# Kernel optimization log

Hardware: AMD Instinct MI355X
Metric: run time of the kernel (lower is better)

Reference implementation:

```python
import jax, jax.numpy as jnp
import numpy as np

B, S, E, H = 256, 512, 128, 256


def setup_inputs() -> dict:
    key = jax.random.key(0)
    ks = jax.random.split(key, 20)
    s = lambda *sh: 1.0 / np.sqrt(sh[-1])
    inp = jax.random.uniform(ks[0], (B, S, 2), dtype=jnp.float32)
    W_emb = jax.random.normal(ks[1], (E, 2), jnp.float32) * 0.5
    dec_input = jax.random.normal(ks[2], (E,), jnp.float32) * 0.1
    # encoder LSTM (input E -> hidden H), pytorch gate order i,f,g,o
    enc_Wih = jax.random.normal(ks[3], (4 * H, E), jnp.float32) * s(E)
    enc_Whh = jax.random.normal(ks[4], (4 * H, H), jnp.float32) * s(H)
    enc_bih = jnp.zeros((4 * H,), jnp.float32)
    enc_bhh = jnp.zeros((4 * H,), jnp.float32)
    # process block LSTM (input E -> hidden H)
    pb_Wih = jax.random.normal(ks[5], (4 * H, E), jnp.float32) * s(E)
    pb_Whh = jax.random.normal(ks[6], (4 * H, H), jnp.float32) * s(H)
    pb_bih = jnp.zeros((4 * H,), jnp.float32)
    pb_bhh = jnp.zeros((4 * H,), jnp.float32)
    # attention: W_q Linear(H,H), W_ref Conv1d(H,H,1), v vector
    Wq = jax.random.normal(ks[7], (H, H), jnp.float32) * s(H)
    bq = jnp.zeros((H,), jnp.float32)
    Wref = jax.random.normal(ks[8], (H, H), jnp.float32) * s(H)
    bref = jnp.zeros((H,), jnp.float32)
    V = jax.random.normal(ks[9], (H,), jnp.float32) * s(H)
    # decoder: Linear(H,H,bias=False) -> ReLU -> Linear(H,1,bias=False)
    Wd1 = jax.random.normal(ks[10], (H, H), jnp.float32) * s(H)
    Wd2 = jax.random.normal(ks[11], (1, H), jnp.float32) * s(H)
    return dict(inp=inp, W_emb=W_emb, dec_input=dec_input,
                enc_Wih=enc_Wih, enc_Whh=enc_Whh, enc_bih=enc_bih, enc_bhh=enc_bhh,
                pb_Wih=pb_Wih, pb_Whh=pb_Whh, pb_bih=pb_bih, pb_bhh=pb_bhh,
                Wq=Wq, bq=bq, Wref=Wref, bref=bref, V=V, Wd1=Wd1, Wd2=Wd2)


def _lstm_step(Whh):
    def step(carry, x_proj):
        h, c = carry
        g = x_proj + h @ Whh.T  # [B,4H]
        i, f, gg, o = jnp.split(g, 4, axis=-1)
        c = jax.nn.sigmoid(f) * c + jax.nn.sigmoid(i) * jnp.tanh(gg)
        h = jax.nn.sigmoid(o) * jnp.tanh(c)
        return (h, c), h
    return step


def reference(inp, W_emb, dec_input,
              enc_Wih, enc_Whh, enc_bih, enc_bhh,
              pb_Wih, pb_Whh, pb_bih, pb_bhh,
              Wq, bq, Wref, bref, V, Wd1, Wd2):
    b, seq, _ = inp.shape
    hdim = enc_Whh.shape[1]
    emb = inp @ W_emb.T  # [B,S,E]

    # ---- encoder LSTM over the sequence ----
    x_proj = emb @ enc_Wih.T + enc_bih + enc_bhh  # [B,S,4H]
    h0 = jnp.zeros((b, hdim), inp.dtype)
    c0 = jnp.zeros((b, hdim), inp.dtype)
    (h, c), hs = jax.lax.scan(_lstm_step(enc_Whh), (h0, c0),
                              jnp.swapaxes(x_proj, 0, 1))
    enc_out = jnp.swapaxes(hs, 0, 1)  # [B,S,H]

    # ---- process block: seq steps of single-step LSTM with constant input ----
    xp = dec_input @ pb_Wih.T + pb_bih + pb_bhh  # [4H]
    xp = jnp.broadcast_to(xp, (b, xp.shape[0]))
    step = _lstm_step(pb_Whh)
    (h, c), _ = jax.lax.scan(lambda carry, _: (step(carry, xp)[0], None),
                             (h, c), None, length=seq)

    # ---- attention (glimpse) with final hidden; inner iter loop is idempotent ----
    ref = enc_out @ Wref.T + bref            # [B,S,H]  (Conv1d kernel=1)
    q = h @ Wq.T + bq                        # [B,H]
    u = jnp.tanh(ref + q[:, None, :]) @ V    # [B,S]
    align = jax.nn.softmax(u, axis=-1)
    g_l = jnp.einsum('bs,bsh->bh', align, enc_out)  # glimpse [B,H]

    # ---- decoder head ----
    out = (jax.nn.relu(g_l @ Wd1.T)) @ Wd2.T  # [B,1]
    return out.squeeze(-1)
```

## Files before the change

### kernel.cpp

```cpp
#include <hip/hip_runtime.h>

#define B_ 256
#define S_ 512
#define E_ 128
#define H_ 256
#define FH_ 1024
#define HROW 264

typedef __bf16 bf16x8 __attribute__((ext_vector_type(8)));
typedef float f32x4 __attribute__((ext_vector_type(4)));
typedef unsigned short u16x4 __attribute__((ext_vector_type(4)));
typedef unsigned short u16x8 __attribute__((ext_vector_type(8)));
typedef unsigned long long u64_;

__device__ __forceinline__ unsigned short f2bf(float f) {
  union { float f; unsigned int u; } a; a.f = f;
  unsigned int u = a.u;
  u += 0x7fffu + ((u >> 16) & 1u);
  return (unsigned short)(u >> 16);
}
__device__ __forceinline__ float bf2f(unsigned short v) {
  union { unsigned int u; float f; } a; a.u = ((unsigned int)v) << 16;
  return a.f;
}
__device__ __forceinline__ float rcp_(float x) {
  float r;
  asm("v_rcp_f32 %0, %1" : "=v"(r) : "v"(x));
  return r;
}
__device__ __forceinline__ float sigm(float x) { return rcp_(1.f + __expf(-x)); }
__device__ __forceinline__ float tanh_(float x) {
  return 1.f - 2.f * rcp_(__expf(2.f * x) + 1.f);
}
__device__ __forceinline__ unsigned int cvt_pk_bf16(float lo, float hi) {
  unsigned int r;
  asm("v_cvt_pk_bf16_f32 %0, %1, %2" : "=v"(r) : "v"(lo), "v"(hi));
  return r;
}

#define OFF_ENC    ((size_t)0)
#define OFF_WHHE   ((size_t)67108864)
#define OFF_WHHP   ((size_t)67633152)
#define OFF_WREF   ((size_t)68157440)
#define OFF_MENC   ((size_t)68288512)
#define OFF_BIASE  ((size_t)68296704)
#define OFF_XPV    ((size_t)68300800)
#define OFF_FLAGS  ((size_t)68304896)
#define OFF_HX     ((size_t)68305920)
#define OFF_HFIN   ((size_t)68568064)
#define OFF_QBUF   ((size_t)68830208)
#define OFF_UBUF   ((size_t)69092352)

__global__ void k0_prep(const float* __restrict__ eWih, const float* __restrict__ eWhh,
                        const float* __restrict__ ebih, const float* __restrict__ ebhh,
                        const float* __restrict__ pWih, const float* __restrict__ pWhh,
                        const float* __restrict__ pbih, const float* __restrict__ pbhh,
                        const float* __restrict__ W_emb, const float* __restrict__ dec_in,
                        const float* __restrict__ Wref,
                        unsigned short* __restrict__ WhhE, unsigned short* __restrict__ WhhP,
                        unsigned short* __restrict__ Wrefb,
                        float* __restrict__ Menc, float* __restrict__ biasE,
                        float* __restrict__ xpv,
                        unsigned int* __restrict__ flags, float* __restrict__ ubuf) {
  int gid = blockIdx.x * blockDim.x + threadIdx.x;
  int NT = gridDim.x * blockDim.x;
  for (int i = gid; i < FH_ * H_; i += NT) {
    WhhE[i] = f2bf(eWhh[i]);
    WhhP[i] = f2bf(pWhh[i]);
  }
  for (int i = gid; i < H_ * H_; i += NT) Wrefb[i] = f2bf(Wref[i]);
  for (int i = gid; i < B_ * S_; i += NT) ubuf[i] = 0.f;
  if (gid < 256) flags[gid] = 0u;
  if (gid < FH_) {
    int n = gid;
    float m0 = 0.f, m1 = 0.f, xs = 0.f;
    for (int e = 0; e < E_; ++e) {
      float w = eWih[n * E_ + e];
      m0 += w * W_emb[e * 2 + 0];
      m1 += w * W_emb[e * 2 + 1];
      xs += pWih[n * E_ + e] * dec_in[e];
    }
    Menc[n * 2 + 0] = m0;
    Menc[n * 2 + 1] = m1;
    biasE[n] = ebih[n] + ebhh[n];
    xpv[n] = xs + pbih[n] + pbhh[n];
  }
}

__launch_bounds__(512)
__attribute__((amdgpu_waves_per_eu(2, 2)))
__global__ void k1_lstm(const float* __restrict__ inp,
                        const unsigned short* __restrict__ WhhE,
                        const unsigned short* __restrict__ WhhP,
                        const float* __restrict__ Menc, const float* __restrict__ biasE,
                        const float* __restrict__ xpv,
                        unsigned short* __restrict__ enc_out,
                        unsigned short* __restrict__ hx,
                        unsigned int* __restrict__ flags,
                        float* __restrict__ hfin) {
  __shared__ unsigned short hbuf[16 * HROW];
  __shared__ float xin[16][2];
  const int tid = threadIdx.x;
  const int wave = tid >> 6, lane = tid & 63, quad = lane >> 4, l16 = lane & 15;
  const int blk = blockIdx.x;
  const int grp = (blk & 7) | ((blk >> 4) << 3);
  const int half = (blk >> 3) & 1;
  const int kloc = (wave << 4) | l16;
  const int kcol = half * 128 + kloc;

  for (int i = tid; i < 16 * HROW; i += 512) hbuf[i] = 0;
  if (tid < 32) xin[tid >> 1][tid & 1] = inp[((grp * 16 + (tid >> 1)) * S_ + 0) * 2 + (tid & 1)];

  float c[4] = {0.f, 0.f, 0.f, 0.f};
  float hreg[4] = {0.f, 0.f, 0.f, 0.f};
  f32x4 W00, W01, W02, W03, W04, W05, W06, W07;
  f32x4 W10, W11, W12, W13, W14, W15, W16, W17;
  f32x4 W20, W21, W22, W23, W24, W25, W26, W27;
  f32x4 W30, W31, W32, W33, W34, W35, W36, W37;
  float m0c[4], m1c[4], bc[4];
  unsigned int* myflag = flags + grp * 2 + half;
  unsigned int* pflag = flags + grp * 2 + (1 - half);
  const f32x4 z4 = {0.f, 0.f, 0.f, 0.f};
  __syncthreads();

  int t = 0;
#pragma unroll 1
  for (int phase = 0; phase < 2; ++phase) {
    const unsigned short* W = phase ? WhhP : WhhE;
#define WLOAD(g)                                                        \
    {                                                                   \
      const unsigned short* wp = W + ((g) * 256 + kcol) * H_ + quad * 8; \
      W##g##0 = *(const f32x4*)(wp + 0 * 32);                           \
      W##g##1 = *(const f32x4*)(wp + 1 * 32);                           \
      W##g##2 = *(const f32x4*)(wp + 2 * 32);                           \
      W##g##3 = *(const f32x4*)(wp + 3 * 32);                           \
      W##g##4 = *(const f32x4*)(wp + 4 * 32);                           \
      W##g##5 = *(const f32x4*)(wp + 5 * 32);                           \
      W##g##6 = *(const f32x4*)(wp + 6 * 32);                           \
      W##g##7 = *(const f32x4*)(wp + 7 * 32);                           \
    }
    WLOAD(0) WLOAD(1) WLOAD(2) WLOAD(3)
#undef WLOAD
    asm volatile(""
                 : "+v"(W00), "+v"(W01), "+v"(W02), "+v"(W03),
                   "+v"(W04), "+v"(W05), "+v"(W06), "+v"(W07),
                   "+v"(W10), "+v"(W11), "+v"(W12), "+v"(W13),
                   "+v"(W14), "+v"(W15), "+v"(W16), "+v"(W17),
                   "+v"(W20), "+v"(W21), "+v"(W22), "+v"(W23),
                   "+v"(W24), "+v"(W25), "+v"(W26), "+v"(W27),
                   "+v"(W30), "+v"(W31), "+v"(W32), "+v"(W33),
                   "+v"(W34), "+v"(W35), "+v"(W36), "+v"(W37));
#pragma unroll
    for (int gg = 0; gg < 4; ++gg) {
      int n = gg * 256 + kcol;
      if (phase == 0) {
        m0c[gg] = Menc[n * 2 + 0]; m1c[gg] = Menc[n * 2 + 1]; bc[gg] = biasE[n];
      } else {
        m0c[gg] = 0.f; m1c[gg] = 0.f; bc[gg] = xpv[n];
      }
    }
#pragma unroll 1
    for (int step = 0; step < 512; ++step, ++t) {
      float xpre = 0.f;
      if (phase == 0 && tid < 32) {
        int sN = (step < 511) ? step + 1 : 511;
        xpre = inp[((grp * 16 + (tid >> 1)) * S_ + sN) * 2 + (tid & 1)];
      }
      f32x4 acc0 = z4, acc1 = z4, acc2 = z4, acc3 = z4;
#define MSTEP(kt)                                                              \
      {                                                                        \
        bf16x8 Af = *(const bf16x8*)(hbuf + l16 * HROW + kt * 32 + quad * 8);  \
        acc0 = __builtin_amdgcn_mfma_f32_16x16x32_bf16(                        \
            Af, __builtin_bit_cast(bf16x8, W0##kt), acc0, 0, 0, 0);            \
        acc1 = __builtin_amdgcn_mfma_f32_16x16x32_bf16(                        \
            Af, __builtin_bit_cast(bf16x8, W1##kt), acc1, 0, 0, 0);            \
        acc2 = __builtin_amdgcn_mfma_f32_16x16x32_bf16(                        \
            Af, __builtin_bit_cast(bf16x8, W2##kt), acc2, 0, 0, 0);            \
        acc3 = __builtin_amdgcn_mfma_f32_16x16x32_bf16(                        \
            Af, __builtin_bit_cast(bf16x8, W3##kt), acc3, 0, 0, 0);            \
      }
      MSTEP(0) MSTEP(1) MSTEP(2) MSTEP(3) MSTEP(4) MSTEP(5) MSTEP(6) MSTEP(7)
#undef MSTEP
      float hv[4];
#pragma unroll
      for (int r = 0; r < 4; ++r) {
        int bl = quad * 4 + r;
        float x0 = xin[bl][0], x1 = xin[bl][1];
        float gi = acc0[r] + x0 * m0c[0] + x1 * m1c[0] + bc[0];
        float gf = acc1[r] + x0 * m0c[1] + x1 * m1c[1] + bc[1];
        float gc = acc2[r] + x0 * m0c[2] + x1 * m1c[2] + bc[2];
        float go = acc3[r] + x0 * m0c[3] + x1 * m1c[3] + bc[3];
        float cn = sigm(gf) * c[r] + sigm(gi) * tanh_(gc);
        c[r] = cn;
        hv[r] = sigm(go) * tanh_(cn);
        hreg[r] = hv[r];
      }
      unsigned int pkA = cvt_pk_bf16(hv[0], hv[1]);
      unsigned int pkB = cvt_pk_bf16(hv[2], hv[3]);
      unsigned short hb[4];
      hb[0] = (unsigned short)pkA; hb[1] = (unsigned short)(pkA >> 16);
      hb[2] = (unsigned short)pkB; hb[3] = (unsigned short)(pkB >> 16);
      if (phase == 0) {
#pragma unroll
        for (int r = 0; r < 4; ++r)
          enc_out[(((size_t)(grp * 16 + quad * 4 + r) * S_ + step)) * H_ + kcol] = hb[r];
      }
      {
        unsigned short* hxs = hx + ((size_t)((t & 1) * 32 + grp * 2 + half)) * 2048;
        u64_ pack = (u64_)pkA | ((u64_)pkB << 32);
        __hip_atomic_store((u64_*)(hxs + kloc * 16 + quad * 4), pack,
                           __ATOMIC_RELAXED, __HIP_MEMORY_SCOPE_AGENT);
      }
      __syncthreads();
      if (phase == 0 && tid < 32) xin[tid >> 1][tid & 1] = xpre;
      if (tid == 0) {
        __hip_atomic_store(myflag, (unsigned int)(t + 1), __ATOMIC_RELAXED,
                           __HIP_MEMORY_SCOPE_AGENT);
        while (__hip_atomic_load(pflag, __ATOMIC_RELAXED, __HIP_MEMORY_SCOPE_AGENT) <
               (unsigned int)(t + 1)) {
          __builtin_amdgcn_s_sleep(1);
        }
      }
      __syncthreads();
#pragma unroll
      for (int r = 0; r < 4; ++r) hbuf[(quad * 4 + r) * HROW + kcol] = hb[r];
      {
        const unsigned short* ph = hx + ((size_t)((t & 1) * 32 + grp * 2 + (1 - half))) * 2048;
        u64_ pv = __hip_atomic_load((const u64_*)(ph + tid * 4), __ATOMIC_RELAXED,
                                    __HIP_MEMORY_SCOPE_AGENT);
        int kp = tid >> 2, r0 = (tid & 3) * 4;
        unsigned short* dst = hbuf + (1 - half) * 128 + kp;
        dst[(size_t)(r0 + 0) * HROW] = (unsigned short)(pv);
        dst[(size_t)(r0 + 1) * HROW] = (unsigned short)(pv >> 16);
        dst[(size_t)(r0 + 2) * HROW] = (unsigned short)(pv >> 32);
        dst[(size_t)(r0 + 3) * HROW] = (unsigned short)(pv >> 48);
      }
      __syncthreads();
    }
  }
#pragma unroll
  for (int r = 0; r < 4; ++r)
    hfin[(grp * 16 + quad * 4 + r) * H_ + kcol] = hreg[r];
}

__global__ void k1b_q(const float* __restrict__ hfin, const float* __restrict__ Wq,
                      const float* __restrict__ bq, float* __restrict__ qbuf) {
  __shared__ float hl[H_];
  int b = blockIdx.x, j = threadIdx.x;
  hl[j] = hfin[b * H_ + j];
  __syncthreads();
  float s = bq[j];
  const float* w = Wq + j * H_;
  for (int k = 0; k < H_; ++k) s += hl[k] * w[k];
  qbuf[b * H_ + j] = s;
}

__launch_bounds__(512)
__global__ void k2_att(const unsigned short* __restrict__ enc_out,
                       const unsigned short* __restrict__ Wrefb,
                       const float* __restrict__ qbuf, const float* __restrict__ bref,
                       const float* __restrict__ V, float* __restrict__ ubuf) {
  __shared__ unsigned short Bs[128 * HROW];
  __shared__ float qs[128], Vs[128];
  int tid = threadIdx.x;
  int wave = tid >> 6, lane = tid & 63, quad = lane >> 4, l16 = lane & 15;
  int rowblk = blockIdx.x >> 1, nb = blockIdx.x & 1;
  int b = rowblk >> 2;
  {
    int nl = tid >> 2, seg = tid & 3;
    const unsigned short* src = Wrefb + (nb * 128 + nl) * H_ + seg * 64;
    unsigned short* dst = Bs + nl * HROW + seg * 64;
#pragma unroll
    for (int i = 0; i < 8; ++i) *(u16x8*)(dst + i * 8) = *(const u16x8*)(src + i * 8);
  }
  if (tid < 128) {
    int j = nb * 128 + tid;
    qs[tid] = qbuf[b * H_ + j] + bref[j];
    Vs[tid] = V[j];
  }
  __syncthreads();
  int rw = rowblk * 128 + wave * 16 + l16;
  const f32x4 z4 = {0.f, 0.f, 0.f, 0.f};
  f32x4 acc[8];
#pragma unroll
  for (int kt = 0; kt < 8; ++kt) {
    bf16x8 af = *(const bf16x8*)(enc_out + (size_t)rw * H_ + kt * 32 + quad * 8);
#pragma unroll
    for (int nt = 0; nt < 8; ++nt) {
      bf16x8 bfr = *(const bf16x8*)(Bs + (nt * 16 + l16) * HROW + kt * 32 + quad * 8);
      acc[nt] = __builtin_amdgcn_mfma_f32_16x16x32_bf16(af, bfr, (kt == 0) ? z4 : acc[nt],
                                                        0, 0, 0);
    }
  }
  float part[4] = {0.f, 0.f, 0.f, 0.f};
#pragma unroll
  for (int nt = 0; nt < 8; ++nt) {
    float qv = qs[nt * 16 + l16], vv = Vs[nt * 16 + l16];
#pragma unroll
    for (int r = 0; r < 4; ++r) part[r] += tanh_(acc[nt][r] + qv) * vv;
  }
#pragma unroll
  for (int m = 1; m < 16; m <<= 1) {
#pragma unroll
    for (int r = 0; r < 4; ++r) part[r] += __shfl_xor(part[r], m, 64);
  }
  if (l16 == 0) {
    int s0 = (rowblk & 3) * 128 + wave * 16 + quad * 4;
#pragma unroll
    for (int r = 0; r < 4; ++r) atomicAdd(&ubuf[b * S_ + s0 + r], part[r]);
  }
}

__global__ void k3_head(const float* __restrict__ ubuf,
                        const unsigned short* __restrict__ enc_out,
                        const float* __restrict__ Wd1, const float* __restrict__ Wd2,
                        float* __restrict__ out) {
  __shared__ float sm[512];
  __shared__ float red[256];
  __shared__ float gl[256];
  int b = blockIdx.x, tid = threadIdx.x;
  float u0 = ubuf[b * S_ + tid], u1 = ubuf[b * S_ + 256 + tid];
  red[tid] = fmaxf(u0, u1);
  __syncthreads();
  for (int s = 128; s > 0; s >>= 1) {
    if (tid < s) red[tid] = fmaxf(red[tid], red[tid + s]);
    __syncthreads();
  }
  float mx = red[0];
  __syncthreads();
  float e0 = __expf(u0 - mx), e1 = __expf(u1 - mx);
  red[tid] = e0 + e1;
  __syncthreads();
  for (int s = 128; s > 0; s >>= 1) {
    if (tid < s) red[tid] += red[tid + s];
    __syncthreads();
  }
  float inv = 1.f / red[0];
  sm[tid] = e0 * inv;
  sm[256 + tid] = e1 * inv;
  __syncthreads();
  float g = 0.f;
  const unsigned short* eo = enc_out + (size_t)b * S_ * H_ + tid;
  for (int s = 0; s < S_; ++s) g += sm[s] * bf2f(eo[(size_t)s * H_]);
  gl[tid] = g;
  __syncthreads();
  float y = 0.f;
  const float* w = Wd1 + tid * H_;
  for (int j = 0; j < H_; ++j) y += w[j] * gl[j];
  y = fmaxf(y, 0.f) * Wd2[tid];
  red[tid] = y;
  __syncthreads();
  for (int s = 128; s > 0; s >>= 1) {
    if (tid < s) red[tid] += red[tid + s];
    __syncthreads();
  }
  if (tid == 0) out[b] = red[0];
}

extern "C" void kernel_launch(void* const* d_in, const int* in_sizes, int n_in,
                              void* d_out, int out_size, void* d_ws, size_t ws_size,
                              hipStream_t stream) {
  (void)in_sizes; (void)n_in; (void)out_size; (void)ws_size;
  const float* inp    = (const float*)d_in[0];
  const float* W_emb  = (const float*)d_in[1];
  const float* dec_in = (const float*)d_in[2];
  const float* eWih   = (const float*)d_in[3];
  const float* eWhh   = (const float*)d_in[4];
  const float* ebih   = (const float*)d_in[5];
  const float* ebhh   = (const float*)d_in[6];
  const float* pWih   = (const float*)d_in[7];
  const float* pWhh   = (const float*)d_in[8];
  const float* pbih   = (const float*)d_in[9];
  const float* pbhh   = (const float*)d_in[10];
  const float* Wq     = (const float*)d_in[11];
  const float* bq     = (const float*)d_in[12];
  const float* Wref   = (const float*)d_in[13];
  const float* bref   = (const float*)d_in[14];
  const float* V      = (const float*)d_in[15];
  const float* Wd1    = (const float*)d_in[16];
  const float* Wd2    = (const float*)d_in[17];
  float* out = (float*)d_out;

  char* ws = (char*)d_ws;
  unsigned short* enc_out = (unsigned short*)(ws + OFF_ENC);
  unsigned short* WhhE    = (unsigned short*)(ws + OFF_WHHE);
  unsigned short* WhhP    = (unsigned short*)(ws + OFF_WHHP);
  unsigned short* Wrefb   = (unsigned short*)(ws + OFF_WREF);
  float* Menc  = (float*)(ws + OFF_MENC);
  float* biasE = (float*)(ws + OFF_BIASE);
  float* xpv   = (float*)(ws + OFF_XPV);
  unsigned int* flags = (unsigned int*)(ws + OFF_FLAGS);
  unsigned short* hx  = (unsigned short*)(ws + OFF_HX);
  float* hfin = (float*)(ws + OFF_HFIN);
  float* qbuf = (float*)(ws + OFF_QBUF);
  float* ubuf = (float*)(ws + OFF_UBUF);

  hipLaunchKernelGGL(k0_prep, dim3(256), dim3(256), 0, stream,
                     eWih, eWhh, ebih, ebhh, pWih, pWhh, pbih, pbhh, W_emb, dec_in,
                     Wref, WhhE, WhhP, Wrefb, Menc, biasE, xpv, flags, ubuf);
  hipLaunchKernelGGL(k1_lstm, dim3(32), dim3(512), 0, stream,
                     inp, WhhE, WhhP, Menc, biasE, xpv, enc_out, hx, flags, hfin);
  hipLaunchKernelGGL(k1b_q, dim3(256), dim3(256), 0, stream, hfin, Wq, bq, qbuf);
  hipLaunchKernelGGL(k2_att, dim3(2048), dim3(512), 0, stream,
                     enc_out, Wrefb, qbuf, bref, V, ubuf);
  hipLaunchKernelGGL(k3_head, dim3(256), dim3(256), 0, stream,
                     ubuf, enc_out, Wd1, Wd2, out);
}
```

Measured before the change: 2.641 ms.

## Double-buffer hidden state and use per-wave flags for cross-block LSTM handshake

The LSTM recurrence now keeps two shared-memory copies of the hidden-state tile and of the input scratch, indexed by step parity. This lets each wave write its next-step hidden values locally before synchronising. The single block-wide flag, polled by thread 0 between two barriers, is replaced by one flag per wave. Each wave publishes its slice after waiting for its own global stores, then spins only on the matching wave of the partner block. This removes two block barriers per step from the latency-bound 1024-step loop. The cost is a flags array eight times larger, plus more polling traffic from every wave instead of one thread.

New measurement: 5.742 ms. +117.5%, slower.

```diff
diff --git a/kernel.cpp b/kernel.cpp
--- a/kernel.cpp
+++ b/kernel.cpp
@@ -98,8 +98,8 @@
                         unsigned short* __restrict__ hx,
                         unsigned int* __restrict__ flags,
                         float* __restrict__ hfin) {
-  __shared__ unsigned short hbuf[16 * HROW];
-  __shared__ float xin[16][2];
+  __shared__ unsigned short hbuf[2][16 * HROW];
+  __shared__ float xin[2][16][2];
   const int tid = threadIdx.x;
   const int wave = tid >> 6, lane = tid & 63, quad = lane >> 4, l16 = lane & 15;
   const int blk = blockIdx.x;
@@ -108,8 +108,9 @@
   const int kloc = (wave << 4) | l16;
   const int kcol = half * 128 + kloc;
 
-  for (int i = tid; i < 16 * HROW; i += 512) hbuf[i] = 0;
-  if (tid < 32) xin[tid >> 1][tid & 1] = inp[((grp * 16 + (tid >> 1)) * S_ + 0) * 2 + (tid & 1)];
+  for (int i = tid; i < 16 * HROW; i += 512) hbuf[0][i] = 0;
+  if (tid < 32)
+    xin[0][tid >> 1][tid & 1] = inp[((grp * 16 + (tid >> 1)) * S_ + 0) * 2 + (tid & 1)];
 
   float c[4] = {0.f, 0.f, 0.f, 0.f};
   float hreg[4] = {0.f, 0.f, 0.f, 0.f};
@@ -118,8 +119,8 @@
   f32x4 W20, W21, W22, W23, W24, W25, W26, W27;
   f32x4 W30, W31, W32, W33, W34, W35, W36, W37;
   float m0c[4], m1c[4], bc[4];
-  unsigned int* myflag = flags + grp * 2 + half;
-  unsigned int* pflag = flags + grp * 2 + (1 - half);
+  unsigned int* myflagw = flags + ((grp * 2 + half) << 3) + wave;
+  unsigned int* pflagw = flags + ((grp * 2 + (1 - half)) << 3) + wave;
   const f32x4 z4 = {0.f, 0.f, 0.f, 0.f};
   __syncthreads();
 
@@ -161,23 +162,24 @@
     }
 #pragma unroll 1
     for (int step = 0; step < 512; ++step, ++t) {
+      const int cur = t & 1, nxt = cur ^ 1;
       float xpre = 0.f;
       if (phase == 0 && tid < 32) {
         int sN = (step < 511) ? step + 1 : 511;
         xpre = inp[((grp * 16 + (tid >> 1)) * S_ + sN) * 2 + (tid & 1)];
       }
       f32x4 acc0 = z4, acc1 = z4, acc2 = z4, acc3 = z4;
-#define MSTEP(kt)                                                              \
-      {                                                                        \
-        bf16x8 Af = *(const bf16x8*)(hbuf + l16 * HROW + kt * 32 + quad * 8);  \
-        acc0 = __builtin_amdgcn_mfma_f32_16x16x32_bf16(                        \
-            Af, __builtin_bit_cast(bf16x8, W0##kt), acc0, 0, 0, 0);            \
-        acc1 = __builtin_amdgcn_mfma_f32_16x16x32_bf16(                        \
-            Af, __builtin_bit_cast(bf16x8, W1##kt), acc1, 0, 0, 0);            \
-        acc2 = __builtin_amdgcn_mfma_f32_16x16x32_bf16(                        \
-            Af, __builtin_bit_cast(bf16x8, W2##kt), acc2, 0, 0, 0);            \
-        acc3 = __builtin_amdgcn_mfma_f32_16x16x32_bf16(                        \
-            Af, __builtin_bit_cast(bf16x8, W3##kt), acc3, 0, 0, 0);            \
+#define MSTEP(kt)                                                                  \
+      {                                                                            \
+        bf16x8 Af = *(const bf16x8*)(&hbuf[cur][0] + l16 * HROW + kt * 32 + quad * 8); \
+        acc0 = __builtin_amdgcn_mfma_f32_16x16x32_bf16(                            \
+            Af, __builtin_bit_cast(bf16x8, W0##kt), acc0, 0, 0, 0);                \
+        acc1 = __builtin_amdgcn_mfma_f32_16x16x32_bf16(                            \
+            Af, __builtin_bit_cast(bf16x8, W1##kt), acc1, 0, 0, 0);                \
+        acc2 = __builtin_amdgcn_mfma_f32_16x16x32_bf16(                            \
+            Af, __builtin_bit_cast(bf16x8, W2##kt), acc2, 0, 0, 0);                \
+        acc3 = __builtin_amdgcn_mfma_f32_16x16x32_bf16(                            \
+            Af, __builtin_bit_cast(bf16x8, W3##kt), acc3, 0, 0, 0);                \
       }
       MSTEP(0) MSTEP(1) MSTEP(2) MSTEP(3) MSTEP(4) MSTEP(5) MSTEP(6) MSTEP(7)
 #undef MSTEP
@@ -185,7 +187,7 @@
 #pragma unroll
       for (int r = 0; r < 4; ++r) {
         int bl = quad * 4 + r;
-        float x0 = xin[bl][0], x1 = xin[bl][1];
+        float x0 = xin[cur][bl][0], x1 = xin[cur][bl][1];
         float gi = acc0[r] + x0 * m0c[0] + x1 * m1c[0] + bc[0];
         float gf = acc1[r] + x0 * m0c[1] + x1 * m1c[1] + bc[1];
         float gc = acc2[r] + x0 * m0c[2] + x1 * m1c[2] + bc[2];
@@ -206,30 +208,30 @@
           enc_out[(((size_t)(grp * 16 + quad * 4 + r) * S_ + step)) * H_ + kcol] = hb[r];
       }
       {
-        unsigned short* hxs = hx + ((size_t)((t & 1) * 32 + grp * 2 + half)) * 2048;
+        unsigned short* hxs = hx + ((size_t)(nxt * 32 + grp * 2 + half)) * 2048;
         u64_ pack = (u64_)pkA | ((u64_)pkB << 32);
         __hip_atomic_store((u64_*)(hxs + kloc * 16 + quad * 4), pack,
                            __ATOMIC_RELAXED, __HIP_MEMORY_SCOPE_AGENT);
       }
-      __syncthreads();
-      if (phase == 0 && tid < 32) xin[tid >> 1][tid & 1] = xpre;
-      if (tid == 0) {
-        __hip_atomic_store(myflag, (unsigned int)(t + 1), __ATOMIC_RELAXED,
+#pragma unroll
+      for (int r = 0; r < 4; ++r) hbuf[nxt][(quad * 4 + r) * HROW + kcol] = hb[r];
+      if (phase == 0 && tid < 32) xin[nxt][tid >> 1][tid & 1] = xpre;
+      asm volatile("s_waitcnt vmcnt(0)" ::: "memory");
+      if (lane == 0)
+        __hip_atomic_store(myflagw, (unsigned int)(t + 1), __ATOMIC_RELAXED,
                            __HIP_MEMORY_SCOPE_AGENT);
-        while (__hip_atomic_load(pflag, __ATOMIC_RELAXED, __HIP_MEMORY_SCOPE_AGENT) <
-               (unsigned int)(t + 1)) {
+      {
+        const unsigned int target = (unsigned int)(t + 1);
+        while (__hip_atomic_load(pflagw, __ATOMIC_RELAXED, __HIP_MEMORY_SCOPE_AGENT) <
+               target) {
           __builtin_amdgcn_s_sleep(1);
         }
-      }
-      __syncthreads();
-#pragma unroll
-      for (int r = 0; r < 4; ++r) hbuf[(quad * 4 + r) * HROW + kcol] = hb[r];
-      {
-        const unsigned short* ph = hx + ((size_t)((t & 1) * 32 + grp * 2 + (1 - half))) * 2048;
+        const unsigned short* ph =
+            hx + ((size_t)(nxt * 32 + grp * 2 + (1 - half))) * 2048;
         u64_ pv = __hip_atomic_load((const u64_*)(ph + tid * 4), __ATOMIC_RELAXED,
                                     __HIP_MEMORY_SCOPE_AGENT);
         int kp = tid >> 2, r0 = (tid & 3) * 4;
-        unsigned short* dst = hbuf + (1 - half) * 128 + kp;
+        unsigned short* dst = &hbuf[nxt][0] + (1 - half) * 128 + kp;
         dst[(size_t)(r0 + 0) * HROW] = (unsigned short)(pv);
         dst[(size_t)(r0 + 1) * HROW] = (unsigned short)(pv >> 16);
         dst[(size_t)(r0 + 2) * HROW] = (unsigned short)(pv >> 32);
```
